# Kernel optimization log

Hardware: AMD Instinct MI355X
Metric: run time of the kernel (lower is better)

## Reference

```python
import jax, jax.numpy as jnp
import numpy as np

NEG = -1e30  # log-space 'zero'
BLANK = 0


def setup_inputs() -> dict:
    key = jax.random.key(0)
    k1, k2, k3, k4, k5, k6 = jax.random.split(key, 6)
    B, T, D, V, L = 16, 500, 256, 5000, 50
    encoder_out = jax.random.normal(k1, (B, T, D), dtype=jnp.float32)
    encoder_out_lens = jax.random.randint(k2, (B,), 400, T + 1, dtype=jnp.int32)
    y = jax.random.randint(k3, (B, L), 1, V, dtype=jnp.int32)  # blank=0 excluded
    y_lens = jax.random.randint(k4, (B,), 30, L + 1, dtype=jnp.int32)
    W = jax.random.normal(k5, (V, D), dtype=jnp.float32) * (1.0 / np.sqrt(D))
    b = jax.random.normal(k6, (V,), dtype=jnp.float32) * 0.01
    return {"encoder_out": encoder_out, "encoder_out_lens": encoder_out_lens,
            "y": y, "y_lens": y_lens, "W": W, "b": b}


def _ctc_neg_logp(lp, ext, skip, enc_lens, y_lens):
    # lp: [T,B,V] log-probs; ext: [B,S] extended label seq (blank interleaved)
    T, B, V = lp.shape
    S = ext.shape[1]
    # per-frame log-probs of the extended labels: [T,B,S]
    lp_ext = jnp.take_along_axis(lp, jnp.broadcast_to(ext[None], (T, B, S)), axis=2)

    end_idx = jnp.stack([2 * y_lens, 2 * y_lens - 1], axis=1)  # [B,2]

    def end_of(alpha):
        vals = jnp.take_along_axis(alpha, end_idx, axis=1)  # [B,2]
        return jnp.logaddexp(vals[:, 0], vals[:, 1])

    alpha0 = jnp.full((B, S), NEG, lp.dtype)
    alpha0 = alpha0.at[:, 0].set(lp_ext[0, :, 0])
    alpha0 = alpha0.at[:, 1].set(lp_ext[0, :, 1])

    pad1 = jnp.full((B, 1), NEG, lp.dtype)
    pad2 = jnp.full((B, 2), NEG, lp.dtype)

    def step(alpha, lp_t):
        prev1 = jnp.concatenate([pad1, alpha[:, :-1]], axis=1)
        prev2 = jnp.concatenate([pad2, alpha[:, :-2]], axis=1)
        m = jnp.logaddexp(alpha, prev1)
        m = jnp.logaddexp(m, jnp.where(skip, prev2, NEG))
        new = m + lp_t
        return new, end_of(new)

    _, ends_rest = jax.lax.scan(step, alpha0, lp_ext[1:])  # [T-1,B]
    ends = jnp.concatenate([end_of(alpha0)[None], ends_rest], axis=0)  # [T,B]
    final = jnp.take_along_axis(ends, (enc_lens - 1)[None, :], axis=0)[0]  # [B]
    return -final


def reference(encoder_out, encoder_out_lens, y, y_lens, W, b):
    # dropout is identity here (deterministic/eval reference)
    B = encoder_out.shape[0]
    logits = jnp.einsum('btd,vd->btv', encoder_out, W) + b  # [B,T,V]
    lp = jax.nn.log_softmax(logits, axis=-1)
    lp = jnp.transpose(lp, (1, 0, 2))  # [T,B,V]

    L = y.shape[1]
    S = 2 * L + 1
    ext = jnp.zeros((B, S), dtype=y.dtype).at[:, 1::2].set(y)  # blank-interleaved
    s_idx = jnp.arange(S)
    ext_m2 = jnp.concatenate([jnp.zeros((B, 2), ext.dtype), ext[:, :-2]], axis=1)
    skip = (s_idx[None, :] >= 2) & (ext != ext_m2) & (ext != BLANK)

    neg_logp = _ctc_neg_logp(lp, ext, skip, encoder_out_lens, y_lens)
    loss = jnp.sum(neg_logp) / B  # CTCLoss(reduction='sum') / batch_size
    return loss
```

## Files before the change

### kernel.cpp

```cpp
#include <hip/hip_runtime.h>
#include <hip/hip_bf16.h>

#define NEG (-1e30f)
#define M_ROWS 8000
#define N_COLS 5000
#define K_DIM  256
#define T_LEN  500
#define T_PAD  512
#define B_SZ   16
#define L_LAB  50
#define LDS_STR 72
#define DP_STR  516
#define LOG2E   1.4426950408889634f
#define LN2     0.6931471805599453f

typedef _Float16 half8  __attribute__((ext_vector_type(8)));
typedef _Float16 half4v __attribute__((ext_vector_type(4)));
typedef float    floatx4 __attribute__((ext_vector_type(4)));

__device__ __forceinline__ float fexp2(float x) {
#if defined(__has_builtin)
#if __has_builtin(__builtin_amdgcn_exp2f)
  return __builtin_amdgcn_exp2f(x);
#else
  return __expf(x * LN2);
#endif
#else
  return __expf(x * LN2);
#endif
}
__device__ __forceinline__ float flog2(float x) {
#if defined(__has_builtin)
#if __has_builtin(__builtin_amdgcn_logf)
  return __builtin_amdgcn_logf(x);
#else
  return __logf(x) * LOG2E;
#endif
#else
  return __logf(x) * LOG2E;
#endif
}
__device__ __forceinline__ float wave_shr1(float x, float fill) {
#if defined(__has_builtin)
#if __has_builtin(__builtin_amdgcn_update_dpp)
  int r = __builtin_amdgcn_update_dpp(__float_as_int(fill), __float_as_int(x),
                                      0x138 , 0xf, 0xf, false);
  return __int_as_float(r);
#else
  return __shfl_up(x, 1);
#endif
#else
  return __shfl_up(x, 1);
#endif
}

__global__ void k_f2h2(const float* __restrict__ enc, const float* __restrict__ W,
                       _Float16* __restrict__ ench, _Float16* __restrict__ wh,
                       float* z, float* psum) {
  int i = blockIdx.x * blockDim.x + threadIdx.x;
  if (i == 0) z[0] = 0.0f;
  if (i < M_ROWS) psum[i] = 0.0f;
  if (i < 512000) {
    float4 v = ((const float4*)enc)[i];
    half4v o = {(_Float16)v.x, (_Float16)v.y, (_Float16)v.z, (_Float16)v.w};
    ((half4v*)ench)[i] = o;
  } else {
    int k = i - 512000;
    if (k < 320000) {
      float4 v = ((const float4*)W)[k];
      half4v o = {(_Float16)v.x, (_Float16)v.y, (_Float16)v.z, (_Float16)v.w};
      ((half4v*)wh)[k] = o;
    }
  }
}

__global__ __launch_bounds__(256) void k_gemm_lse(
    const _Float16* __restrict__ A, const _Float16* __restrict__ Bm,
    const float* __restrict__ bias, const int* __restrict__ y,
    float* __restrict__ psum, float* __restrict__ lgT) {
  __shared__ _Float16 As[128 * LDS_STR];
  __shared__ _Float16 Bs[128 * LDS_STR];

  const int tid = threadIdx.x;
  const int lane = tid & 63;
  const int wid = tid >> 6;
  const int wave_m = wid & 1, wave_n = wid >> 1;
  const int l15 = lane & 15, quad = lane >> 4;
  const int m0 = blockIdx.y * 128, n0 = blockIdx.x * 128;

  floatx4 acc[4][4];
  floatx4 zz = {0.f, 0.f, 0.f, 0.f};
  #pragma unroll
  for (int mi = 0; mi < 4; ++mi)
    #pragma unroll
    for (int ni = 0; ni < 4; ++ni) acc[mi][ni] = zz;

  for (int kk = 0; kk < K_DIM; kk += 64) {
    #pragma unroll
    for (int r = 0; r < 4; ++r) {
      int flat = r * 256 + tid;
      int row = flat >> 3, c8 = flat & 7;
      int ga = m0 + row; if (ga > M_ROWS - 1) ga = M_ROWS - 1;
      int4 av = *(const int4*)(A + (size_t)ga * K_DIM + kk + c8 * 8);
      *(int4*)(As + row * LDS_STR + c8 * 8) = av;
      int gb = n0 + row; if (gb > N_COLS - 1) gb = N_COLS - 1;
      int4 bv = *(const int4*)(Bm + (size_t)gb * K_DIM + kk + c8 * 8);
      *(int4*)(Bs + row * LDS_STR + c8 * 8) = bv;
    }
    __syncthreads();
    #pragma unroll
    for (int ko = 0; ko < 64; ko += 32) {
      half8 af[4], bf[4];
      #pragma unroll
      for (int mi = 0; mi < 4; ++mi)
        af[mi] = *(const half8*)(As + (wave_m * 64 + mi * 16 + l15) * LDS_STR + ko + quad * 8);
      #pragma unroll
      for (int ni = 0; ni < 4; ++ni)
        bf[ni] = *(const half8*)(Bs + (wave_n * 64 + ni * 16 + l15) * LDS_STR + ko + quad * 8);
      #pragma unroll
      for (int mi = 0; mi < 4; ++mi)
        #pragma unroll
        for (int ni = 0; ni < 4; ++ni)
          acc[mi][ni] = __builtin_amdgcn_mfma_f32_16x16x32_f16(af[mi], bf[ni], acc[mi][ni], 0, 0, 0);
    }
    __syncthreads();
  }

  float bvv[4]; bool cok[4];
  #pragma unroll
  for (int ni = 0; ni < 4; ++ni) {
    int col = n0 + wave_n * 64 + ni * 16 + l15;
    cok[ni] = (col < N_COLS);
    bvv[ni] = cok[ni] ? bias[col] : 0.f;
  }

  const int nbase = n0 + wave_n * 64;
  const int mbase = m0 + wave_m * 64;
  int b_lo = mbase / T_LEN;
  int b_hi = (mbase + 63) / T_LEN;
  if (b_hi > B_SZ - 1) b_hi = B_SZ - 1;
  for (int b = b_lo; b <= b_hi; ++b) {
    int v_l = 0x40000000;
    if (lane <= 50) v_l = (lane == 0) ? 0 : y[b * L_LAB + lane - 1];
    int dv_l = v_l - nbase;
    unsigned long long mask = __ballot(dv_l >= 0 && dv_l < 64);
    while (mask) {
      int j = (int)__builtin_ctzll(mask);
      mask &= mask - 1;
      int dv = __shfl(dv_l, j);
      int ni = dv >> 4;
      float bb = bvv[0];
      bb = (ni == 1) ? bvv[1] : bb;
      bb = (ni == 2) ? bvv[2] : bb;
      bb = (ni == 3) ? bvv[3] : bb;
      if ((dv & 15) == l15) {
        #pragma unroll
        for (int mi = 0; mi < 4; ++mi) {
          #pragma unroll
          for (int r = 0; r < 4; ++r) {
            float val = acc[mi][0][r];
            val = (ni == 1) ? acc[mi][1][r] : val;
            val = (ni == 2) ? acc[mi][2][r] : val;
            val = (ni == 3) ? acc[mi][3][r] : val;
            int grow = mbase + mi * 16 + quad * 4 + r;
            int t = grow - b * T_LEN;
            if (t >= 0 && t < T_LEN && grow < M_ROWS)
              lgT[((size_t)b * 51 + j) * T_PAD + t] = val + bb;
          }
        }
      }
    }
  }

  #pragma unroll
  for (int mi = 0; mi < 4; ++mi) {
    #pragma unroll
    for (int r = 0; r < 4; ++r) {
      int grow = mbase + mi * 16 + quad * 4 + r;
      float se = 0.f;
      se += cok[0] ? fexp2((acc[mi][0][r] + bvv[0]) * LOG2E) : 0.f;
      se += cok[1] ? fexp2((acc[mi][1][r] + bvv[1]) * LOG2E) : 0.f;
      se += cok[2] ? fexp2((acc[mi][2][r] + bvv[2]) * LOG2E) : 0.f;
      se += cok[3] ? fexp2((acc[mi][3][r] + bvv[3]) * LOG2E) : 0.f;
      #pragma unroll
      for (int d = 1; d < 16; d <<= 1) se += __shfl_xor(se, d);
      if (l15 == 0 && grow < M_ROWS) atomicAdd(&psum[grow], se);
    }
  }
}

__global__ __launch_bounds__(256) void k_dp(
    const float* __restrict__ lgT, const float* __restrict__ psum,
    const int* __restrict__ enc_lens, const int* __restrict__ y,
    const int* __restrict__ y_lens, float* __restrict__ out) {
  __shared__ float sA[51 * DP_STR];
  __shared__ float sRed[5];
  const int b = blockIdx.x, tid = threadIdx.x;
  const int Tb = enc_lens[b], yl = y_lens[b];

  const float* g = lgT + (size_t)b * 51 * T_PAD;
  #pragma unroll
  for (int k = 0; k < 26; ++k) {
    int idx = tid + k * 256;
    if (idx < 51 * 128) {
      int row = idx >> 7, c4 = (idx & 127) << 2;
      float4 v = *(const float4*)(g + (size_t)row * T_PAD + c4);
      float4 s = {v.x * LOG2E, v.y * LOG2E, v.z * LOG2E, v.w * LOG2E};
      *(float4*)(sA + row * DP_STR + c4) = s;
    }
  }

  float sl2 = 0.f;
  for (int t = tid; t < Tb; t += 256) sl2 += flog2(psum[b * T_LEN + t]);
  #pragma unroll
  for (int d = 1; d < 64; d <<= 1) sl2 += __shfl_xor(sl2, d);
  if ((tid & 63) == 0) sRed[1 + (tid >> 6)] = sl2;
  __syncthreads();
  const float slse = LN2 * (sRed[1] + sRed[2] + sRed[3] + sRed[4]);

  if (tid < 64) {
    const int i = tid;
    const int jj = (i + 1 < 50) ? (i + 1) : 50;
    const float* bl = sA;
    const float* ow = sA + jj * DP_STR;
    const bool v0 = (i <= 50), v1 = (i <= 49);
    const bool lane0 = (i == 0);
    const bool skip1 = (i >= 1 && i <= 49) && (y[b * L_LAB + i] != y[b * L_LAB + i - 1]);

    float4 A0 = *(const float4*)(bl + 0),  A1 = *(const float4*)(ow + 0);
    float4 B0 = *(const float4*)(bl + 4),  B1 = *(const float4*)(ow + 4);
    float4 C0 = *(const float4*)(bl + 8),  C1 = *(const float4*)(ow + 8);
    float4 D0 = *(const float4*)(bl + 12), D1 = *(const float4*)(ow + 12);
    const float4 n4 = {NEG, NEG, NEG, NEG};
    if (!v1) { A1 = n4; B1 = n4; C1 = n4; D1 = n4; }

    float a0 = lane0 ? A0.x : NEG;
    float a1 = lane0 ? A1.x : NEG;

    auto step = [&](float l0r, float l1) {
      float l0 = v0 ? l0r : NEG;
      float p1 = wave_shr1(a1, NEG);
      p1 = lane0 ? NEG : p1;
      float th = skip1 ? p1 : NEG;
      float m0 = fmaxf(a0, p1);
      float na0 = m0 + flog2(fexp2(a0 - m0) + fexp2(p1 - m0)) + l0;
      float m1 = fmaxf(fmaxf(a1, a0), th);
      float na1 = m1 + flog2(fexp2(a1 - m1) + fexp2(a0 - m1) + fexp2(th - m1)) + l1;
      a0 = na0; a1 = na1;
    };

    step(A0.y, A1.y);
    step(A0.z, A1.z);
    step(A0.w, A1.w);

    float4 c0 = B0, c1 = B1, n0v = C0, n1v = C1, nn0 = D0, nn1 = D1;
    int t = 4;
    while (t + 4 <= Tb) {
      float4 p0 = *(const float4*)(bl + t + 12);
      float4 p1v = *(const float4*)(ow + t + 12);
      if (!v1) p1v = n4;
      step(c0.x, c1.x);
      step(c0.y, c1.y);
      step(c0.z, c1.z);
      step(c0.w, c1.w);
      c0 = n0v; c1 = n1v; n0v = nn0; n1v = nn1; nn0 = p0; nn1 = p1v;
      t += 4;
    }
    if (t < Tb) { step(c0.x, c1.x); ++t; }
    if (t < Tb) { step(c0.y, c1.y); ++t; }
    if (t < Tb) { step(c0.z, c1.z); ++t; }

    float ea = __shfl(a0, yl);
    float eb = __shfl(a1, yl - 1);
    if (lane0) {
      float m = fmaxf(ea, eb);
      float fin = LN2 * (m + flog2(fexp2(ea - m) + fexp2(eb - m)));
      atomicAdd(out, (slse - fin) * (1.0f / (float)B_SZ));
    }
  }
}

extern "C" void kernel_launch(void* const* d_in, const int* in_sizes, int n_in,
                              void* d_out, int out_size, void* d_ws, size_t ws_size,
                              hipStream_t stream) {
  (void)in_sizes; (void)n_in; (void)out_size; (void)ws_size;
  const float* enc      = (const float*)d_in[0];
  const int*   enc_lens = (const int*)d_in[1];
  const int*   y        = (const int*)d_in[2];
  const int*   y_lens   = (const int*)d_in[3];
  const float* W        = (const float*)d_in[4];
  const float* bias     = (const float*)d_in[5];
  float* out = (float*)d_out;

  char* ws = (char*)d_ws;
  _Float16* ench = (_Float16*)(ws + 0);
  _Float16* wh   = (_Float16*)(ws + 4096000);
  float* psum    = (float*)(ws + 6656000);
  float* lgT     = (float*)(ws + 6688000);

  k_f2h2<<<3250, 256, 0, stream>>>(enc, W, ench, wh, out, psum);
  k_gemm_lse<<<dim3(40, 63), 256, 0, stream>>>(ench, wh, bias, y, psum, lgT);
  k_dp<<<16, 256, 0, stream>>>(lgT, psum, enc_lens, y, y_lens, out);
}
```

Measured before the change: 185.3 us.

## Use direct global-to-LDS loads and XCD-aware block remapping in GEMM

Replaces register-staged tile loads with global_load_lds direct transfers into unpadded LDS tiles. Flattens the 2D grid and remaps block indices so consecutive tiles cluster per XCD for better L2 reuse. This removes VGPR staging and load instructions. Dropping the LDS padding may introduce bank conflicts on fragment reads.

```diff
diff --git a/kernel.cpp b/kernel.cpp
--- a/kernel.cpp
+++ b/kernel.cpp
@@ -9,7 +9,6 @@
 #define T_PAD  512
 #define B_SZ   16
 #define L_LAB  50
-#define LDS_STR 72
 #define DP_STR  516
 #define LOG2E   1.4426950408889634f
 #define LN2     0.6931471805599453f
@@ -52,6 +51,13 @@
 #else
   return __shfl_up(x, 1);
 #endif
+}
+
+__device__ __forceinline__ void gload_lds16(const _Float16* g, _Float16* l) {
+  __builtin_amdgcn_global_load_lds(
+      (const __attribute__((address_space(1))) void*)g,
+      (__attribute__((address_space(3))) void*)l,
+      16, 0, 0);
 }
 
 __global__ void k_f2h2(const float* __restrict__ enc, const float* __restrict__ W,
@@ -78,15 +84,19 @@
     const _Float16* __restrict__ A, const _Float16* __restrict__ Bm,
     const float* __restrict__ bias, const int* __restrict__ y,
     float* __restrict__ psum, float* __restrict__ lgT) {
-  __shared__ _Float16 As[128 * LDS_STR];
-  __shared__ _Float16 Bs[128 * LDS_STR];
+  __shared__ _Float16 As[128 * 64];
+  __shared__ _Float16 Bs[128 * 64];
 
   const int tid = threadIdx.x;
   const int lane = tid & 63;
   const int wid = tid >> 6;
   const int wave_m = wid & 1, wave_n = wid >> 1;
   const int l15 = lane & 15, quad = lane >> 4;
-  const int m0 = blockIdx.y * 128, n0 = blockIdx.x * 128;
+
+  const int flat = blockIdx.x;
+  const int wg = (flat & 7) * 315 + (flat >> 3);
+  const int n0 = (wg % 40) * 128;
+  const int m0 = (wg / 40) * 128;
 
   floatx4 acc[4][4];
   floatx4 zz = {0.f, 0.f, 0.f, 0.f};
@@ -95,17 +105,18 @@
     #pragma unroll
     for (int ni = 0; ni < 4; ++ni) acc[mi][ni] = zz;
 
+  const int lrow = lane >> 3;
+  const int co = (lane & 7) * 8;
+
+  #pragma unroll
   for (int kk = 0; kk < K_DIM; kk += 64) {
     #pragma unroll
-    for (int r = 0; r < 4; ++r) {
-      int flat = r * 256 + tid;
-      int row = flat >> 3, c8 = flat & 7;
-      int ga = m0 + row; if (ga > M_ROWS - 1) ga = M_ROWS - 1;
-      int4 av = *(const int4*)(A + (size_t)ga * K_DIM + kk + c8 * 8);
-      *(int4*)(As + row * LDS_STR + c8 * 8) = av;
-      int gb = n0 + row; if (gb > N_COLS - 1) gb = N_COLS - 1;
-      int4 bv = *(const int4*)(Bm + (size_t)gb * K_DIM + kk + c8 * 8);
-      *(int4*)(Bs + row * LDS_STR + c8 * 8) = bv;
+    for (int q = 0; q < 4; ++q) {
+      const int r = wid * 32 + q * 8 + lrow;
+      int ga = m0 + r; if (ga > M_ROWS - 1) ga = M_ROWS - 1;
+      int gb = n0 + r; if (gb > N_COLS - 1) gb = N_COLS - 1;
+      gload_lds16(A + (size_t)ga * K_DIM + kk + co, As + (wid * 32 + q * 8) * 64);
+      gload_lds16(Bm + (size_t)gb * K_DIM + kk + co, Bs + (wid * 32 + q * 8) * 64);
     }
     __syncthreads();
     #pragma unroll
@@ -113,10 +124,10 @@
       half8 af[4], bf[4];
       #pragma unroll
       for (int mi = 0; mi < 4; ++mi)
-        af[mi] = *(const half8*)(As + (wave_m * 64 + mi * 16 + l15) * LDS_STR + ko + quad * 8);
+        af[mi] = *(const half8*)(As + (wave_m * 64 + mi * 16 + l15) * 64 + ko + quad * 8);
       #pragma unroll
       for (int ni = 0; ni < 4; ++ni)
-        bf[ni] = *(const half8*)(Bs + (wave_n * 64 + ni * 16 + l15) * LDS_STR + ko + quad * 8);
+        bf[ni] = *(const half8*)(Bs + (wave_n * 64 + ni * 16 + l15) * 64 + ko + quad * 8);
       #pragma unroll
       for (int mi = 0; mi < 4; ++mi)
         #pragma unroll
@@ -299,6 +310,6 @@
   float* lgT     = (float*)(ws + 6688000);
 
   k_f2h2<<<3250, 256, 0, stream>>>(enc, W, ench, wh, out, psum);
-  k_gemm_lse<<<dim3(40, 63), 256, 0, stream>>>(ench, wh, bias, y, psum, lgT);
+  k_gemm_lse<<<2520, 256, 0, stream>>>(ench, wh, bias, y, psum, lgT);
   k_dp<<<16, 256, 0, stream>>>(lgT, psum, enc_lens, y, y_lens, out);
 }
```

After: 189.5 us. 1.02x slower.
